# Kernel tuning notes

Hardware: AMD Instinct MI355X
Metric: run time of the kernel (lower is better)

Reference implementation:

```python
import jax, jax.numpy as jnp
import numpy as np

EPS = 1e-5

def conv3d(x, w):
    # x: [B,C,D,H,W], w: [O,I,3,3,3], stride 1, padding 1 (size preserving)
    return jax.lax.conv_general_dilated(
        x, w, window_strides=(1, 1, 1),
        padding=((1, 1), (1, 1), (1, 1)),
        dimension_numbers=('NCDHW', 'OIDHW', 'NCDHW'))

def deconv3d(x, w):
    # ConvTranspose3d(k=3, s=1, p=1) == conv3d with spatially flipped kernel, in/out swapped
    # torch ConvTranspose3d weight layout: [in, out, kD, kH, kW]
    wc = jnp.flip(w, axis=(2, 3, 4)).transpose(1, 0, 2, 3, 4)
    return conv3d(x, wc)

def batchnorm(x, bn):
    # bn: [4, C] rows = (gamma, beta, running_mean, running_var); inference mode
    g, b, m, v = bn[0], bn[1], bn[2], bn[3]
    scale = g * jax.lax.rsqrt(v + EPS)
    shift = b - m * scale
    return x * scale[None, :, None, None, None] + shift[None, :, None, None, None]

def qrnn_scan(Z, F, reverse):
    # gated linear recurrence h_t = f_t*h_{t-1} + (1-f_t)*z_t over depth axis (dim 2)
    Zs = jnp.moveaxis(Z, 2, 0)  # [D,B,C,H,W]
    Fs = jnp.moveaxis(F, 2, 0)
    def step(h, zf):
        z, f = zf
        h = f * h + (1.0 - f) * z
        return h, h
    h0 = jnp.zeros_like(Zs[0])  # h=None in torch == h=0 since f*0 vanishes
    _, hs = jax.lax.scan(step, h0, (Zs, Fs), reverse=reverse)
    return jnp.moveaxis(hs, 0, 2)

def qrnn_layer(x, w, bn, hidden, reverse, upsample, transpose):
    if upsample:
        # nn.Upsample(scale_factor=(1,2,2)) nearest
        x = jnp.repeat(jnp.repeat(x, 2, axis=3), 2, axis=4)
    g = deconv3d(x, w) if transpose else conv3d(x, w)
    g = batchnorm(g, bn)
    Z, F = g[:, :hidden], g[:, hidden:]
    return qrnn_scan(jnp.tanh(Z), jax.nn.sigmoid(F), reverse)

def setup_inputs():
    key = jax.random.key(0)
    ks = jax.random.split(key, 12)
    B, D = 4, 31
    x = jax.random.normal(ks[0], (B, 64, D, 32, 32), jnp.float32)
    xs2 = jax.random.normal(ks[1], (B, 32, D, 64, 64), jnp.float32)
    xs1 = jax.random.normal(ks[2], (B, 32, D, 64, 64), jnp.float32)
    xs0 = jax.random.normal(ks[3], (B, 16, D, 128, 128), jnp.float32)
    def wconv(k, shape):
        fan_in = shape[1] * 27
        return jax.random.normal(k, shape, jnp.float32) / np.float32(np.sqrt(fan_in))
    # layer0: UpsampleConv3d 64 -> 32 hidden (gates 64): Conv3d weight [64,64,3,3,3]
    w0 = wconv(ks[4], (64, 64, 3, 3, 3))
    # layer1: DeConv3D 32 -> 32 hidden (gates 64): ConvTranspose weight [in=32,out=64,3,3,3]
    w1 = wconv(ks[5], (32, 64, 3, 3, 3))
    # layer2: UpsampleConv3d 32 -> 16 hidden (gates 32): Conv3d weight [32,32,3,3,3]
    w2 = wconv(ks[6], (32, 32, 3, 3, 3))
    # layer3: DeConv3D 16 -> 16 hidden (gates 32): ConvTranspose weight [16,32,3,3,3]
    w3 = wconv(ks[7], (16, 32, 3, 3, 3))
    def mkbn(k, c):
        k1, k2, k3, k4 = jax.random.split(k, 4)
        return jnp.stack([
            jax.random.uniform(k1, (c,), jnp.float32, 0.5, 1.5),   # gamma
            jax.random.normal(k2, (c,), jnp.float32) * 0.1,        # beta
            jax.random.normal(k3, (c,), jnp.float32) * 0.1,        # running mean
            jax.random.uniform(k4, (c,), jnp.float32, 0.5, 1.5)])  # running var
    bn0 = mkbn(ks[8], 64)
    bn1 = mkbn(ks[9], 64)
    bn2 = mkbn(ks[10], 32)
    bn3 = mkbn(ks[11], 32)
    return dict(x=x, xs0=xs0, xs1=xs1, xs2=xs2,
                w0=w0, w1=w1, w2=w2, w3=w3,
                bn0=bn0, bn1=bn1, bn2=bn2, bn3=bn3)

def reference(x, xs0, xs1, xs2, w0, w1, w2, w3, bn0, bn1, bn2, bn3):
    # QRNN3DDecoder.forward with has_ad=True, reverse=False; scan direction alternates.
    # xs are popped last-first: xs2, xs1, xs0.
    h = qrnn_layer(x, w0, bn0, 32, False, True, False)          # upsample conv -> [B,32,D,64,64]
    h = qrnn_layer(h + xs2, w1, bn1, 32, True, False, True)     # deconv        -> [B,32,D,64,64]
    h = qrnn_layer(h + xs1, w2, bn2, 16, False, True, False)    # upsample conv -> [B,16,D,128,128]
    h = qrnn_layer(h + xs0, w3, bn3, 16, True, False, True)     # deconv        -> [B,16,D,128,128]
    return h
```

## Files before the change

kernel.cpp:

```cpp
#include <hip/hip_runtime.h>
#include <math.h>

#define BB 4
#define DD 31

typedef _Float16 half8 __attribute__((ext_vector_type(8)));
typedef float f32x4 __attribute__((ext_vector_type(4)));

__device__ __forceinline__ int swz(int b) { return b ^ (((b >> 7) & 7) << 4); }

__device__ __forceinline__ half8 ldswz(const _Float16* lin, int byteoff) {
    return *(const half8*)((const char*)lin + swz(byteoff));
}

__device__ __forceinline__ float fast_tanh(float y) {
    float e = __expf(2.f * y);
    return 1.f - 2.f * __builtin_amdgcn_rcpf(e + 1.f);
}
__device__ __forceinline__ float fast_sigmoid(float y) {
    return __builtin_amdgcn_rcpf(1.f + __expf(-y));
}


__global__ void bnprep(const float* __restrict__ bn, int C, float* __restrict__ sh) {
    int c = threadIdx.x;
    if (c >= C) return;
    float g = bn[c], b = bn[C + c], m = bn[2 * C + c], v = bn[3 * C + c];
    sh[c] = b - m * (g * rsqrtf(v + 1e-5f));
}

__global__ void wprep(const float* __restrict__ src, const float* __restrict__ bn,
                      _Float16* __restrict__ dst, int CIN, int COUT, int KS, int tr) {
    int idx = blockIdx.x * 256 + threadIdx.x;
    int total = KS * 32 * COUT;
    if (idx >= total) return;
    int ki = idx % 32;
    int co = (idx / 32) % COUT;
    int ko = idx / (32 * COUT);
    int k = ko * 32 + ki;
    float v = 0.f;
    if (k < 27 * CIN) {
        int tap = k / CIN, ci = k % CIN;
        v = tr ? src[((size_t)ci * COUT + co) * 27 + (26 - tap)]
               : src[((size_t)co * CIN + ci) * 27 + tap];
        v *= bn[co] * rsqrtf(bn[3 * COUT + co] + 1e-5f);
    }
    dst[((size_t)ko * COUT + co) * 32 + ki] = (_Float16)v;
}

__global__ void wprep_up(const float* __restrict__ src, const float* __restrict__ bn,
                         _Float16* __restrict__ dst, int CIN, int COUT) {
    const int KS = 12 * CIN / 32;
    int idx = blockIdx.x * 256 + threadIdx.x;
    int total = 4 * KS * 32 * COUT;
    if (idx >= total) return;
    int ki = idx % 32;
    int co = (idx / 32) % COUT;
    int ko = (idx / (32 * COUT)) % KS;
    int par = idx / (32 * COUT * KS);
    int k = ko * 32 + ki;
    int ci = k % CIN, tap = k / CIN;
    int kd = tap >> 2, ih = (tap >> 1) & 1, iw = tap & 1;
    int ph = par >> 1, pw = par & 1;
    const float c[2][2][3] = {{{1, 0, 0}, {0, 1, 1}}, {{1, 1, 0}, {0, 0, 1}}};
    float v = 0.f;
    for (int kh = 0; kh < 3; ++kh)
        for (int kw = 0; kw < 3; ++kw)
            v += c[ph][ih][kh] * c[pw][iw][kw] *
                 src[((size_t)co * CIN + ci) * 27 + kd * 9 + kh * 3 + kw];
    v *= bn[co] * rsqrtf(bn[3 * COUT + co] + 1e-5f);
    dst[(((size_t)par * KS + ko) * COUT + co) * 32 + ki] = (_Float16)v;
}

__global__ __launch_bounds__(256) void xconv(const float* __restrict__ src,
                                             _Float16* __restrict__ dst) {
    int idx = blockIdx.x * 256 + threadIdx.x;
    if (idx >= 4 * 31 * 1024 * 8) return;
    int cb = idx & 7;
    int pos = (idx >> 3) & 1023;
    int bd = idx >> 13;
    int d = bd % 31, b = bd / 31;
    half8 v;
#pragma unroll
    for (int j = 0; j < 8; ++j)
        v[j] = (_Float16)src[(((size_t)b * 64 + cb * 8 + j) * 31 + d) * 1024 + pos];
    *(half8*)(dst + ((size_t)bd * 1024 + pos) * 64 + cb * 8) = v;
}

template <int CIN, int COUT, int S, int KSTEPS>
__global__ __launch_bounds__(256, 2) void conv_mfma(
    const _Float16* __restrict__ inp,
    const _Float16* __restrict__ wq,
    const float* __restrict__ bnsh,
    _Float16* __restrict__ gout) {

    constexpr int IH = 18;
    constexpr int IW = 18;
    constexpr int NCB = COUT / 16;
    constexpr int NC8 = CIN / 8;
    constexpr int PATCH = 3 * IH * IW;

    __shared__ __align__(16) _Float16 lin[PATCH * CIN];

    const int tid = threadIdx.x;
    const int lane = tid & 63;
    const int wv = tid >> 6;
    const int col = lane & 15;
    const int grp = lane >> 4;

    const int w0 = blockIdx.x * 16;
    const int h0 = blockIdx.y * 16;
    const int bz = blockIdx.z;
    const int d = bz % DD;

    const int ibh = h0 - 1;
    const int ibw = w0 - 1;

    for (int idx = tid; idx < PATCH * NC8; idx += 256) {
        int c8 = idx % NC8;
        int pos = idx / NC8;
        int iw = pos % IW, t = pos / IW;
        int ih = t % IH, kd = t / IH;
        int dz = d + kd - 1, gh = ibh + ih, gw = ibw + iw;
        half8 v = {0, 0, 0, 0, 0, 0, 0, 0};
        if ((unsigned)dz < (unsigned)DD && (unsigned)gh < (unsigned)S &&
            (unsigned)gw < (unsigned)S)
            v = *(const half8*)(inp +
                (((size_t)(bz + kd - 1) * S + gh) * S + gw) * CIN + c8 * 8);
        *(half8*)((char*)lin + swz((pos * CIN + c8 * 8) * 2)) = v;
    }
    __syncthreads();

    f32x4 acc[4][NCB];
#pragma unroll
    for (int f = 0; f < 4; ++f)
#pragma unroll
        for (int n = 0; n < NCB; ++n) acc[f][n] = {0.f, 0.f, 0.f, 0.f};

#pragma unroll
    for (int ko = 0; ko < KSTEPS; ++ko) {
        int kd, kh, kw, ci;
        if (CIN >= 32) {
            int tap = (ko * 32) / CIN;
            kd = tap / 9; kh = (tap / 3) % 3; kw = tap % 3;
            ci = (ko * 32) % CIN + grp * 8;
        } else {
            int t0 = (2 * ko < 27) ? 2 * ko : 26;
            int t1 = (2 * ko + 1 < 27) ? 2 * ko + 1 : 26;
            int hi = grp >> 1;
            kd = hi ? t1 / 9 : t0 / 9;
            kh = hi ? (t1 / 3) % 3 : (t0 / 3) % 3;
            kw = hi ? t1 % 3 : t0 % 3;
            ci = (grp & 1) * 8;
        }

        half8 a[4];
        int iw = col + kw;
        int cb = ((kd * IH + wv * 4 + kh) * IW + iw) * CIN + ci;
#pragma unroll
        for (int f = 0; f < 4; ++f)
            a[f] = ldswz(lin, (cb + f * IW * CIN) * 2);

        half8 bfr[NCB];
#pragma unroll
        for (int n = 0; n < NCB; ++n)
            bfr[n] = *(const half8*)(wq + ((ko * COUT + n * 16 + col) * 32 + grp * 8));
#pragma unroll
        for (int f = 0; f < 4; ++f)
#pragma unroll
            for (int n = 0; n < NCB; ++n)
                acc[f][n] = __builtin_amdgcn_mfma_f32_16x16x32_f16(a[f], bfr[n],
                                                                   acc[f][n], 0, 0, 0);
    }

    const size_t obase = (size_t)bz * S * S * COUT;
#pragma unroll
    for (int n = 0; n < NCB; ++n) {
        int co = n * 16 + col;
        float sh = bnsh[co];
#pragma unroll
        for (int f = 0; f < 4; ++f) {
            int h = h0 + wv * 4 + f;
#pragma unroll
            for (int r = 0; r < 4; ++r) {
                int w = w0 + grp * 4 + r;
                float y = acc[f][n][r] + sh;
                float v = (n < NCB / 2) ? fast_tanh(y) : fast_sigmoid(y);
                gout[obase + ((size_t)h * S + w) * COUT + co] = (_Float16)v;
            }
        }
    }
}

template <int CIN, int COUT, int S, int MINW>
__global__ __launch_bounds__(256, MINW) void conv_up(
    const _Float16* __restrict__ inp,
    const _Float16* __restrict__ wqu,
    const float* __restrict__ bnsh,
    _Float16* __restrict__ gout) {

    constexpr int SIN = S / 2;
    constexpr int KS = 12 * CIN / 32;
    constexpr int NCB = COUT / 16;
    constexpr int NC8 = CIN / 8;
    constexpr int IH = 6, IW = 18;
    constexpr int PATCH = 3 * IH * IW;

    __shared__ __align__(16) _Float16 lin[PATCH * CIN];

    const int tid = threadIdx.x;
    const int lane = tid & 63;
    const int wv = tid >> 6;
    const int col = lane & 15;
    const int grp = lane >> 4;
    const int ph = wv >> 1, pw = wv & 1;

    const int bwp = blockIdx.x * 16;
    const int bhp = blockIdx.y * 4;
    const int bz = blockIdx.z;
    const int d = bz % DD;

    for (int idx = tid; idx < PATCH * NC8; idx += 256) {
        int c8 = idx % NC8;
        int pos = idx / NC8;
        int iwp = pos % IW, t = pos / IW;
        int ihp = t % IH, kd = t / IH;
        int dz = d + kd - 1, gh = bhp - 1 + ihp, gw = bwp - 1 + iwp;
        half8 v = {0, 0, 0, 0, 0, 0, 0, 0};
        if ((unsigned)dz < (unsigned)DD && (unsigned)gh < (unsigned)SIN &&
            (unsigned)gw < (unsigned)SIN)
            v = *(const half8*)(inp +
                (((size_t)(bz + kd - 1) * SIN + gh) * SIN + gw) * CIN + c8 * 8);
        *(half8*)((char*)lin + swz((pos * CIN + c8 * 8) * 2)) = v;
    }
    __syncthreads();

    f32x4 acc[4][NCB];
#pragma unroll
    for (int f = 0; f < 4; ++f)
#pragma unroll
        for (int n = 0; n < NCB; ++n) acc[f][n] = {0.f, 0.f, 0.f, 0.f};

    const _Float16* wqp = wqu + (size_t)(ph * 2 + pw) * KS * COUT * 32;

#pragma unroll
    for (int ko = 0; ko < KS; ++ko) {
        int tap = (ko * 32) / CIN;
        int ci = (ko * 32) % CIN + grp * 8;
        int kd = tap >> 2, ih = (tap >> 1) & 1, iwk = tap & 1;

        int lcol = col + iwk + pw;
        int r0 = ih + ph;
        int cb = ((kd * IH + r0) * IW + lcol) * CIN + ci;
        half8 a[4];
#pragma unroll
        for (int f = 0; f < 4; ++f)
            a[f] = ldswz(lin, (cb + f * IW * CIN) * 2);

        half8 bfr[NCB];
#pragma unroll
        for (int n = 0; n < NCB; ++n)
            bfr[n] = *(const half8*)(wqp + ((ko * COUT + n * 16 + col) * 32 + grp * 8));
#pragma unroll
        for (int f = 0; f < 4; ++f)
#pragma unroll
            for (int n = 0; n < NCB; ++n)
                acc[f][n] = __builtin_amdgcn_mfma_f32_16x16x32_f16(a[f], bfr[n],
                                                                   acc[f][n], 0, 0, 0);
    }

    const size_t obase = (size_t)bz * S * S * COUT;
#pragma unroll
    for (int n = 0; n < NCB; ++n) {
        int co = n * 16 + col;
        float sh = bnsh[co];
#pragma unroll
        for (int f = 0; f < 4; ++f) {
            int h = 2 * (bhp + f) + ph;
#pragma unroll
            for (int r = 0; r < 4; ++r) {
                int w = 2 * (bwp + grp * 4 + r) + pw;
                float y = acc[f][n][r] + sh;
                float v = (n < NCB / 2) ? fast_tanh(y) : fast_sigmoid(y);
                gout[obase + ((size_t)h * S + w) * COUT + co] = (_Float16)v;
            }
        }
    }
}

template <int H, int HW, int LAST>
__global__ __launch_bounds__(256) void qscan(
    const _Float16* __restrict__ g, const float* __restrict__ xs,
    _Float16* __restrict__ hout, float* __restrict__ fout, int rev) {
    constexpr int NCB = H / 8;
    int idx = blockIdx.x * 256 + threadIdx.x;
    if (idx >= BB * HW * NCB) return;
    int cb = idx % NCB;
    int hw = (idx / NCB) % HW;
    int b = idx / (NCB * HW);
    int c0 = cb * 8;

    float h[8];
#pragma unroll
    for (int j = 0; j < 8; ++j) h[j] = 0.f;

    for (int t = 0; t < DD; ++t) {
        int d = rev ? (DD - 1 - t) : t;
        const _Float16* gp = g + ((size_t)(b * DD + d) * HW + hw) * (2 * H);
        half8 z8 = *(const half8*)(gp + c0);
        half8 f8 = *(const half8*)(gp + H + c0);
        if (LAST) {
#pragma unroll
            for (int j = 0; j < 8; ++j) {
                float fv = (float)f8[j];
                h[j] = fv * h[j] + (1.f - fv) * (float)z8[j];
                fout[(((size_t)b * H + c0 + j) * DD + d) * HW + hw] = h[j];
            }
        } else {
            half8 o;
#pragma unroll
            for (int j = 0; j < 8; ++j) {
                float fv = (float)f8[j];
                h[j] = fv * h[j] + (1.f - fv) * (float)z8[j];
                o[j] = (_Float16)(h[j] + xs[(((size_t)b * H + c0 + j) * DD + d) * HW + hw]);
            }
            *(half8*)(hout + ((size_t)(b * DD + d) * HW + hw) * H + c0) = o;
        }
    }
}

extern "C" void kernel_launch(void* const* d_in, const int* in_sizes, int n_in,
                              void* d_out, int out_size, void* d_ws, size_t ws_size,
                              hipStream_t stream) {
    const float* x   = (const float*)d_in[0];
    const float* xs0 = (const float*)d_in[1];
    const float* xs1 = (const float*)d_in[2];
    const float* xs2 = (const float*)d_in[3];
    const float* w0  = (const float*)d_in[4];
    const float* w1  = (const float*)d_in[5];
    const float* w2  = (const float*)d_in[6];
    const float* w3  = (const float*)d_in[7];
    const float* bn0 = (const float*)d_in[8];
    const float* bn1 = (const float*)d_in[9];
    const float* bn2 = (const float*)d_in[10];
    const float* bn3 = (const float*)d_in[11];
    float* out = (float*)d_out;

    char* p = (char*)d_ws;
    _Float16* xf = (_Float16*)p;  p += (size_t)124 * 1024 * 64 * 2;
    _Float16* gA = (_Float16*)p;  p += (size_t)124 * 4096 * 64 * 2;
    _Float16* hA = (_Float16*)p;  p += (size_t)124 * 4096 * 32 * 2;
    _Float16* gB = (_Float16*)p;  p += (size_t)124 * 16384 * 32 * 2;
    _Float16* hB = (_Float16*)p;  p += (size_t)124 * 16384 * 16 * 2;
    _Float16* wqu0 = (_Float16*)p; p += (size_t)4 * 24 * 64 * 32 * 2;
    _Float16* wq1  = (_Float16*)p; p += 27 * 64 * 32 * 2;
    _Float16* wqu2 = (_Float16*)p; p += (size_t)4 * 12 * 32 * 32 * 2;
    _Float16* wq3  = (_Float16*)p; p += 14 * 32 * 32 * 2;
    float* sh0 = (float*)p;       p += 64 * 4;
    float* sh1 = (float*)p;       p += 64 * 4;
    float* sh2 = (float*)p;       p += 64 * 4;
    float* sh3 = (float*)p;       p += 64 * 4;

    xconv<<<(4 * 31 * 1024 * 8 + 255) / 256, 256, 0, stream>>>(x, xf);
    wprep_up<<<(4 * 24 * 32 * 64 + 255) / 256, 256, 0, stream>>>(w0, bn0, wqu0, 64, 64);
    wprep<<<(27 * 32 * 64 + 255) / 256, 256, 0, stream>>>(w1, bn1, wq1, 32, 64, 27, 1);
    wprep_up<<<(4 * 12 * 32 * 32 + 255) / 256, 256, 0, stream>>>(w2, bn2, wqu2, 32, 32);
    wprep<<<(14 * 32 * 32 + 255) / 256, 256, 0, stream>>>(w3, bn3, wq3, 16, 32, 14, 1);
    bnprep<<<1, 64, 0, stream>>>(bn0, 64, sh0);
    bnprep<<<1, 64, 0, stream>>>(bn1, 64, sh1);
    bnprep<<<1, 64, 0, stream>>>(bn2, 32, sh2);
    bnprep<<<1, 64, 0, stream>>>(bn3, 32, sh3);

    conv_up<64, 64, 64, 3><<<dim3(2, 8, BB * DD), 256, 0, stream>>>(xf, wqu0, sh0, gA);
    qscan<32, 4096, 0><<<(BB * 4096 * 4 + 255) / 256, 256, 0, stream>>>(gA, xs2, hA, nullptr, 0);

    conv_mfma<32, 64, 64, 27><<<dim3(4, 4, BB * DD), 256, 0, stream>>>(hA, wq1, sh1, gA);
    qscan<32, 4096, 0><<<(BB * 4096 * 4 + 255) / 256, 256, 0, stream>>>(gA, xs1, hA, nullptr, 1);

    conv_up<32, 32, 128, 4><<<dim3(4, 16, BB * DD), 256, 0, stream>>>(hA, wqu2, sh2, gB);
    qscan<16, 16384, 0><<<(BB * 16384 * 2 + 255) / 256, 256, 0, stream>>>(gB, xs0, hB, nullptr, 0);

    conv_mfma<16, 32, 128, 14><<<dim3(8, 8, BB * DD), 256, 0, stream>>>(hB, wq3, sh3, gB);
    qscan<16, 16384, 1><<<(BB * 16384 * 2 + 255) / 256, 256, 0, stream>>>(gB, nullptr, nullptr, out, 1);
}
```

Measured before the change: 567.1 us.

## Fuse QRNN depth scan into conv kernels with rolling depth-plane LDS buffer

Each conv kernel now walks the whole depth axis for its spatial tile and output-channel slice, keeping the recurrent state in registers and applying tanh/sigmoid, the gated recurrence and the skip-add inline. This removes the separate qscan kernels and the round trip of the gate tensors through global memory. Input planes are staged in a 4-slot rolling LDS ring, with the next plane prefetched into registers during the MFMA work. Weights are re-laid out so each block reads only its channel slice. The cost is far fewer blocks per launch (the depth dimension leaves the grid) and a serial dependency across depth, which lowers parallelism and occupancy.

Result: slower. 602.8 us (+6.3%).

```diff
diff --git a/kernel.cpp b/kernel.cpp
--- a/kernel.cpp
+++ b/kernel.cpp
@@ -8,11 +8,12 @@
 typedef float f32x4 __attribute__((ext_vector_type(4)));
 
 __device__ __forceinline__ int swz(int b) { return b ^ (((b >> 7) & 7) << 4); }
-
 __device__ __forceinline__ half8 ldswz(const _Float16* lin, int byteoff) {
     return *(const half8*)((const char*)lin + swz(byteoff));
 }
-
+__device__ __forceinline__ void stswz(_Float16* lin, int byteoff, half8 v) {
+    *(half8*)((char*)lin + swz(byteoff)) = v;
+}
 __device__ __forceinline__ float fast_tanh(float y) {
     float e = __expf(2.f * y);
     return 1.f - 2.f * __builtin_amdgcn_rcpf(e + 1.f);
@@ -30,13 +31,16 @@
 }
 
 __global__ void wprep(const float* __restrict__ src, const float* __restrict__ bn,
-                      _Float16* __restrict__ dst, int CIN, int COUT, int KS, int tr) {
+                      _Float16* __restrict__ dst, int CIN, int COUT, int KS, int CS, int tr) {
     int idx = blockIdx.x * 256 + threadIdx.x;
-    int total = KS * 32 * COUT;
+    int total = CS * KS * 1024;
     if (idx >= total) return;
-    int ki = idx % 32;
-    int co = (idx / 32) % COUT;
-    int ko = idx / (32 * COUT);
+    int ki = idx & 31;
+    int c16 = (idx >> 5) & 15;
+    int n = (idx >> 9) & 1;
+    int ko = (idx >> 10) % KS;
+    int q = idx / (KS * 1024);
+    int co = n * (COUT / 2) + q * 16 + c16;
     int k = ko * 32 + ki;
     float v = 0.f;
     if (k < 27 * CIN) {
@@ -45,19 +49,21 @@
                : src[((size_t)co * CIN + ci) * 27 + tap];
         v *= bn[co] * rsqrtf(bn[3 * COUT + co] + 1e-5f);
     }
-    dst[((size_t)ko * COUT + co) * 32 + ki] = (_Float16)v;
+    dst[idx] = (_Float16)v;
 }
 
 __global__ void wprep_up(const float* __restrict__ src, const float* __restrict__ bn,
-                         _Float16* __restrict__ dst, int CIN, int COUT) {
-    const int KS = 12 * CIN / 32;
+                         _Float16* __restrict__ dst, int CIN, int COUT, int KS, int CS) {
     int idx = blockIdx.x * 256 + threadIdx.x;
-    int total = 4 * KS * 32 * COUT;
+    int total = CS * 4 * KS * 1024;
     if (idx >= total) return;
-    int ki = idx % 32;
-    int co = (idx / 32) % COUT;
-    int ko = (idx / (32 * COUT)) % KS;
-    int par = idx / (32 * COUT * KS);
+    int ki = idx & 31;
+    int c16 = (idx >> 5) & 15;
+    int n = (idx >> 9) & 1;
+    int ko = (idx >> 10) % KS;
+    int par = (idx / (KS * 1024)) & 3;
+    int q = idx / (KS * 4096);
+    int co = n * (COUT / 2) + q * 16 + c16;
     int k = ko * 32 + ki;
     int ci = k % CIN, tap = k / CIN;
     int kd = tap >> 2, ih = (tap >> 1) & 1, iw = tap & 1;
@@ -69,7 +75,7 @@
             v += c[ph][ih][kh] * c[pw][iw][kw] *
                  src[((size_t)co * CIN + ci) * 27 + kd * 9 + kh * 3 + kw];
     v *= bn[co] * rsqrtf(bn[3 * COUT + co] + 1e-5f);
-    dst[(((size_t)par * KS + ko) * COUT + co) * 32 + ki] = (_Float16)v;
+    dst[idx] = (_Float16)v;
 }
 
 __global__ __launch_bounds__(256) void xconv(const float* __restrict__ src,
@@ -87,20 +93,24 @@
     *(half8*)(dst + ((size_t)bd * 1024 + pos) * 64 + cb * 8) = v;
 }
 
-template <int CIN, int COUT, int S, int KSTEPS>
-__global__ __launch_bounds__(256, 2) void conv_mfma(
+template <int CIN, int S, int HID, int KS, int NF, int CS, int REV, int LAST>
+__global__ __launch_bounds__(256, 2) void fconv(
     const _Float16* __restrict__ inp,
     const _Float16* __restrict__ wq,
     const float* __restrict__ bnsh,
-    _Float16* __restrict__ gout) {
-
-    constexpr int IH = 18;
+    const float* __restrict__ xs,
+    _Float16* __restrict__ hout,
+    float* __restrict__ fout) {
+
     constexpr int IW = 18;
-    constexpr int NCB = COUT / 16;
+    constexpr int TH = 4 * NF;
+    constexpr int IHP = TH + 2;
     constexpr int NC8 = CIN / 8;
-    constexpr int PATCH = 3 * IH * IW;
-
-    __shared__ __align__(16) _Float16 lin[PATCH * CIN];
+    constexpr int P8 = IHP * IW * NC8;
+    constexpr int NST = (P8 + 255) / 256;
+    constexpr int PLANEB = IHP * IW * CIN * 2;
+
+    __shared__ __align__(16) _Float16 lin[4 * IHP * IW * CIN];
 
     const int tid = threadIdx.x;
     const int lane = tid & 63;
@@ -109,104 +119,158 @@
     const int grp = lane >> 4;
 
     const int w0 = blockIdx.x * 16;
-    const int h0 = blockIdx.y * 16;
-    const int bz = blockIdx.z;
-    const int d = bz % DD;
-
-    const int ibh = h0 - 1;
-    const int ibw = w0 - 1;
-
-    for (int idx = tid; idx < PATCH * NC8; idx += 256) {
-        int c8 = idx % NC8;
-        int pos = idx / NC8;
-        int iw = pos % IW, t = pos / IW;
-        int ih = t % IH, kd = t / IH;
-        int dz = d + kd - 1, gh = ibh + ih, gw = ibw + iw;
-        half8 v = {0, 0, 0, 0, 0, 0, 0, 0};
-        if ((unsigned)dz < (unsigned)DD && (unsigned)gh < (unsigned)S &&
-            (unsigned)gw < (unsigned)S)
-            v = *(const half8*)(inp +
-                (((size_t)(bz + kd - 1) * S + gh) * S + gw) * CIN + c8 * 8);
-        *(half8*)((char*)lin + swz((pos * CIN + c8 * 8) * 2)) = v;
-    }
+    const int h0 = blockIdx.y * TH;
+    const int b = blockIdx.z / CS;
+    const int q = blockIdx.z % CS;
+    const size_t bbase = (size_t)b * DD;
+
+    const float shz = bnsh[q * 16 + col];
+    const float shf = bnsh[HID + q * 16 + col];
+    const int hc = q * 16 + col;
+    const _Float16* wqb = wq + (size_t)q * KS * 1024;
+
+    auto stage_now = [&](int dz) {
+        int slot = (dz + 8) & 3;
+        for (int idx = tid; idx < P8; idx += 256) {
+            int c8 = idx % NC8;
+            int pos = idx / NC8;
+            int ih = pos / IW, iw = pos % IW;
+            int gh = h0 - 1 + ih, gw = w0 - 1 + iw;
+            half8 v = {0, 0, 0, 0, 0, 0, 0, 0};
+            if ((unsigned)dz < (unsigned)DD && (unsigned)gh < (unsigned)S &&
+                (unsigned)gw < (unsigned)S)
+                v = *(const half8*)(inp + (((bbase + dz) * S + gh) * S + gw) * CIN + c8 * 8);
+            stswz(lin, slot * PLANEB + (pos * CIN + c8 * 8) * 2, v);
+        }
+    };
+
+    constexpr int dir = REV ? -1 : 1;
+    const int d0 = REV ? DD - 1 : 0;
+    stage_now(d0 - dir);
+    stage_now(d0);
+    stage_now(d0 + dir);
     __syncthreads();
 
-    f32x4 acc[4][NCB];
-#pragma unroll
-    for (int f = 0; f < 4; ++f)
-#pragma unroll
-        for (int n = 0; n < NCB; ++n) acc[f][n] = {0.f, 0.f, 0.f, 0.f};
-
-#pragma unroll
-    for (int ko = 0; ko < KSTEPS; ++ko) {
-        int kd, kh, kw, ci;
-        if (CIN >= 32) {
-            int tap = (ko * 32) / CIN;
-            kd = tap / 9; kh = (tap / 3) % 3; kw = tap % 3;
-            ci = (ko * 32) % CIN + grp * 8;
-        } else {
-            int t0 = (2 * ko < 27) ? 2 * ko : 26;
-            int t1 = (2 * ko + 1 < 27) ? 2 * ko + 1 : 26;
-            int hi = grp >> 1;
-            kd = hi ? t1 / 9 : t0 / 9;
-            kh = hi ? (t1 / 3) % 3 : (t0 / 3) % 3;
-            kw = hi ? t1 % 3 : t0 % 3;
-            ci = (grp & 1) * 8;
-        }
-
-        half8 a[4];
-        int iw = col + kw;
-        int cb = ((kd * IH + wv * 4 + kh) * IW + iw) * CIN + ci;
-#pragma unroll
-        for (int f = 0; f < 4; ++f)
-            a[f] = ldswz(lin, (cb + f * IW * CIN) * 2);
-
-        half8 bfr[NCB];
-#pragma unroll
-        for (int n = 0; n < NCB; ++n)
-            bfr[n] = *(const half8*)(wq + ((ko * COUT + n * 16 + col) * 32 + grp * 8));
-#pragma unroll
-        for (int f = 0; f < 4; ++f)
-#pragma unroll
-            for (int n = 0; n < NCB; ++n)
-                acc[f][n] = __builtin_amdgcn_mfma_f32_16x16x32_f16(a[f], bfr[n],
-                                                                   acc[f][n], 0, 0, 0);
-    }
-
-    const size_t obase = (size_t)bz * S * S * COUT;
-#pragma unroll
-    for (int n = 0; n < NCB; ++n) {
-        int co = n * 16 + col;
-        float sh = bnsh[co];
-#pragma unroll
-        for (int f = 0; f < 4; ++f) {
-            int h = h0 + wv * 4 + f;
+    float hst[NF][4];
+#pragma unroll
+    for (int f = 0; f < NF; ++f)
+#pragma unroll
+        for (int r = 0; r < 4; ++r) hst[f][r] = 0.f;
+
+    for (int t = 0; t < DD; ++t) {
+        const int d = d0 + dir * t;
+        const int dzl = d + 2 * dir;
+
+        half8 sv[NST];
+#pragma unroll
+        for (int i = 0; i < NST; ++i) {
+            int idx = tid + i * 256;
+            half8 v = {0, 0, 0, 0, 0, 0, 0, 0};
+            if (idx < P8) {
+                int c8 = idx % NC8;
+                int pos = idx / NC8;
+                int ih = pos / IW, iw = pos % IW;
+                int gh = h0 - 1 + ih, gw = w0 - 1 + iw;
+                if ((unsigned)dzl < (unsigned)DD && (unsigned)gh < (unsigned)S &&
+                    (unsigned)gw < (unsigned)S)
+                    v = *(const half8*)(inp +
+                        (((bbase + dzl) * S + gh) * S + gw) * CIN + c8 * 8);
+            }
+            sv[i] = v;
+        }
+
+        f32x4 acc[NF][2];
+#pragma unroll
+        for (int f = 0; f < NF; ++f) {
+            acc[f][0] = {0.f, 0.f, 0.f, 0.f};
+            acc[f][1] = {0.f, 0.f, 0.f, 0.f};
+        }
+#pragma unroll
+        for (int ko = 0; ko < KS; ++ko) {
+            int kd, kh, kw, ci;
+            if (CIN >= 32) {
+                int tap = (ko * 32) / CIN;
+                kd = tap / 9; kh = (tap / 3) % 3; kw = tap % 3;
+                ci = (ko * 32) % CIN + grp * 8;
+            } else {
+                int t0 = (2 * ko < 27) ? 2 * ko : 26;
+                int t1 = (2 * ko + 1 < 27) ? 2 * ko + 1 : 26;
+                int hi = grp >> 1;
+                kd = hi ? t1 / 9 : t0 / 9;
+                kh = hi ? (t1 / 3) % 3 : (t0 / 3) % 3;
+                kw = hi ? t1 % 3 : t0 % 3;
+                ci = (grp & 1) * 8;
+            }
+            int slot = (d + kd + 7) & 3;
+            int iw = col + kw;
+            half8 a[NF];
+#pragma unroll
+            for (int f = 0; f < NF; ++f)
+                a[f] = ldswz(lin, slot * PLANEB +
+                             (((wv * NF + f + kh) * IW + iw) * CIN + ci) * 2);
+            half8 bf0 = *(const half8*)(wqb + ko * 1024 + col * 32 + grp * 8);
+            half8 bf1 = *(const half8*)(wqb + ko * 1024 + 512 + col * 32 + grp * 8);
+#pragma unroll
+            for (int f = 0; f < NF; ++f) {
+                acc[f][0] = __builtin_amdgcn_mfma_f32_16x16x32_f16(a[f], bf0, acc[f][0], 0, 0, 0);
+                acc[f][1] = __builtin_amdgcn_mfma_f32_16x16x32_f16(a[f], bf1, acc[f][1], 0, 0, 0);
+            }
+        }
+
+        {
+            int slot = (dzl + 8) & 3;
+#pragma unroll
+            for (int i = 0; i < NST; ++i) {
+                int idx = tid + i * 256;
+                if (idx < P8) {
+                    int c8 = idx % NC8;
+                    int pos = idx / NC8;
+                    stswz(lin, slot * PLANEB + (pos * CIN + c8 * 8) * 2, sv[i]);
+                }
+            }
+        }
+
+#pragma unroll
+        for (int f = 0; f < NF; ++f) {
+            int h = h0 + wv * NF + f;
 #pragma unroll
             for (int r = 0; r < 4; ++r) {
                 int w = w0 + grp * 4 + r;
-                float y = acc[f][n][r] + sh;
-                float v = (n < NCB / 2) ? fast_tanh(y) : fast_sigmoid(y);
-                gout[obase + ((size_t)h * S + w) * COUT + co] = (_Float16)v;
-            }
-        }
+                size_t sp = (size_t)h * S + w;
+                float z = fast_tanh(acc[f][0][r] + shz);
+                float fg = fast_sigmoid(acc[f][1][r] + shf);
+                hst[f][r] = fg * hst[f][r] + (1.f - fg) * z;
+                if (LAST) {
+                    fout[(((size_t)b * HID + hc) * DD + d) * ((size_t)S * S) + sp] = hst[f][r];
+                } else {
+                    float xv = xs[(((size_t)b * HID + hc) * DD + d) * ((size_t)S * S) + sp];
+                    hout[((bbase + d) * ((size_t)S * S) + sp) * HID + hc] =
+                        (_Float16)(hst[f][r] + xv);
+                }
+            }
+        }
+        __syncthreads();
     }
 }
 
-template <int CIN, int COUT, int S, int MINW>
-__global__ __launch_bounds__(256, MINW) void conv_up(
+template <int CIN, int S, int HID, int KS, int NF, int CS, int REV, int LAST>
+__global__ __launch_bounds__(256, 2) void fconv_up(
     const _Float16* __restrict__ inp,
-    const _Float16* __restrict__ wqu,
+    const _Float16* __restrict__ wq,
     const float* __restrict__ bnsh,
-    _Float16* __restrict__ gout) {
+    const float* __restrict__ xs,
+    _Float16* __restrict__ hout,
+    float* __restrict__ fout) {
 
     constexpr int SIN = S / 2;
-    constexpr int KS = 12 * CIN / 32;
-    constexpr int NCB = COUT / 16;
+    constexpr int IW = 18;
+    constexpr int IHP = NF + 2;
     constexpr int NC8 = CIN / 8;
-    constexpr int IH = 6, IW = 18;
-    constexpr int PATCH = 3 * IH * IW;
-
-    __shared__ __align__(16) _Float16 lin[PATCH * CIN];
+    constexpr int P8 = IHP * IW * NC8;
+    constexpr int NST = (P8 + 255) / 256;
+    constexpr int PLANEB = IHP * IW * CIN * 2;
+
+    __shared__ __align__(16) _Float16 lin[4 * IHP * IW * CIN];
 
     const int tid = threadIdx.x;
     const int lane = tid & 63;
@@ -216,116 +280,127 @@
     const int ph = wv >> 1, pw = wv & 1;
 
     const int bwp = blockIdx.x * 16;
-    const int bhp = blockIdx.y * 4;
-    const int bz = blockIdx.z;
-    const int d = bz % DD;
-
-    for (int idx = tid; idx < PATCH * NC8; idx += 256) {
-        int c8 = idx % NC8;
-        int pos = idx / NC8;
-        int iwp = pos % IW, t = pos / IW;
-        int ihp = t % IH, kd = t / IH;
-        int dz = d + kd - 1, gh = bhp - 1 + ihp, gw = bwp - 1 + iwp;
-        half8 v = {0, 0, 0, 0, 0, 0, 0, 0};
-        if ((unsigned)dz < (unsigned)DD && (unsigned)gh < (unsigned)SIN &&
-            (unsigned)gw < (unsigned)SIN)
-            v = *(const half8*)(inp +
-                (((size_t)(bz + kd - 1) * SIN + gh) * SIN + gw) * CIN + c8 * 8);
-        *(half8*)((char*)lin + swz((pos * CIN + c8 * 8) * 2)) = v;
-    }
+    const int bhp = blockIdx.y * NF;
+    const int b = blockIdx.z / CS;
+    const int q = blockIdx.z % CS;
+    const size_t bbase = (size_t)b * DD;
+
+    const float shz = bnsh[q * 16 + col];
+    const float shf = bnsh[HID + q * 16 + col];
+    const int hc = q * 16 + col;
+    const _Float16* wqb = wq + ((size_t)(q * 4 + wv) * KS) * 1024;
+
+    auto stage_now = [&](int dz) {
+        int slot = (dz + 8) & 3;
+        for (int idx = tid; idx < P8; idx += 256) {
+            int c8 = idx % NC8;
+            int pos = idx / NC8;
+            int ih = pos / IW, iw = pos % IW;
+            int gh = bhp - 1 + ih, gw = bwp - 1 + iw;
+            half8 v = {0, 0, 0, 0, 0, 0, 0, 0};
+            if ((unsigned)dz < (unsigned)DD && (unsigned)gh < (unsigned)SIN &&
+                (unsigned)gw < (unsigned)SIN)
+                v = *(const half8*)(inp + (((bbase + dz) * SIN + gh) * SIN + gw) * CIN + c8 * 8);
+            stswz(lin, slot * PLANEB + (pos * CIN + c8 * 8) * 2, v);
+        }
+    };
+
+    constexpr int dir = REV ? -1 : 1;
+    const int d0 = REV ? DD - 1 : 0;
+    stage_now(d0 - dir);
+    stage_now(d0);
+    stage_now(d0 + dir);
     __syncthreads();
 
-    f32x4 acc[4][NCB];
-#pragma unroll
-    for (int f = 0; f < 4; ++f)
-#pragma unroll
-        for (int n = 0; n < NCB; ++n) acc[f][n] = {0.f, 0.f, 0.f, 0.f};
-
-    const _Float16* wqp = wqu + (size_t)(ph * 2 + pw) * KS * COUT * 32;
-
-#pragma unroll
-    for (int ko = 0; ko < KS; ++ko) {
-        int tap = (ko * 32) / CIN;
-        int ci = (ko * 32) % CIN + grp * 8;
-        int kd = tap >> 2, ih = (tap >> 1) & 1, iwk = tap & 1;
-
-        int lcol = col + iwk + pw;
-        int r0 = ih + ph;
-        int cb = ((kd * IH + r0) * IW + lcol) * CIN + ci;
-        half8 a[4];
-#pragma unroll
-        for (int f = 0; f < 4; ++f)
-            a[f] = ldswz(lin, (cb + f * IW * CIN) * 2);
-
-        half8 bfr[NCB];
-#pragma unroll
-        for (int n = 0; n < NCB; ++n)
-            bfr[n] = *(const half8*)(wqp + ((ko * COUT + n * 16 + col) * 32 + grp * 8));
-#pragma unroll
-        for (int f = 0; f < 4; ++f)
-#pragma unroll
-            for (int n = 0; n < NCB; ++n)
-                acc[f][n] = __builtin_amdgcn_mfma_f32_16x16x32_f16(a[f], bfr[n],
-                                                                   acc[f][n], 0, 0, 0);
-    }
-
-    const size_t obase = (size_t)bz * S * S * COUT;
-#pragma unroll
-    for (int n = 0; n < NCB; ++n) {
-        int co = n * 16 + col;
-        float sh = bnsh[co];
-#pragma unroll
-        for (int f = 0; f < 4; ++f) {
+    float hst[NF][4];
+#pragma unroll
+    for (int f = 0; f < NF; ++f)
+#pragma unroll
+        for (int r = 0; r < 4; ++r) hst[f][r] = 0.f;
+
+    for (int t = 0; t < DD; ++t) {
+        const int d = d0 + dir * t;
+        const int dzl = d + 2 * dir;
+
+        half8 sv[NST];
+#pragma unroll
+        for (int i = 0; i < NST; ++i) {
+            int idx = tid + i * 256;
+            half8 v = {0, 0, 0, 0, 0, 0, 0, 0};
+            if (idx < P8) {
+                int c8 = idx % NC8;
+                int pos = idx / NC8;
+                int ih = pos / IW, iw = pos % IW;
+                int gh = bhp - 1 + ih, gw = bwp - 1 + iw;
+                if ((unsigned)dzl < (unsigned)DD && (unsigned)gh < (unsigned)SIN &&
+                    (unsigned)gw < (unsigned)SIN)
+                    v = *(const half8*)(inp +
+                        (((bbase + dzl) * SIN + gh) * SIN + gw) * CIN + c8 * 8);
+            }
+            sv[i] = v;
+        }
+
+        f32x4 acc[NF][2];
+#pragma unroll
+        for (int f = 0; f < NF; ++f) {
+            acc[f][0] = {0.f, 0.f, 0.f, 0.f};
+            acc[f][1] = {0.f, 0.f, 0.f, 0.f};
+        }
+#pragma unroll
+        for (int ko = 0; ko < KS; ++ko) {
+            int tap = (ko * 32) / CIN;
+            int ci = (ko * 32) % CIN + grp * 8;
+            int kd = tap >> 2, ihh = (tap >> 1) & 1, iwk = tap & 1;
+            int slot = (d + kd + 7) & 3;
+            int lcol = col + iwk + pw;
+            int row0 = ihh + ph;
+            half8 a[NF];
+#pragma unroll
+            for (int f = 0; f < NF; ++f)
+                a[f] = ldswz(lin, slot * PLANEB +
+                             ((((row0 + f) * IW) + lcol) * CIN + ci) * 2);
+            half8 bf0 = *(const half8*)(wqb + ko * 1024 + col * 32 + grp * 8);
+            half8 bf1 = *(const half8*)(wqb + ko * 1024 + 512 + col * 32 + grp * 8);
+#pragma unroll
+            for (int f = 0; f < NF; ++f) {
+                acc[f][0] = __builtin_amdgcn_mfma_f32_16x16x32_f16(a[f], bf0, acc[f][0], 0, 0, 0);
+                acc[f][1] = __builtin_amdgcn_mfma_f32_16x16x32_f16(a[f], bf1, acc[f][1], 0, 0, 0);
+            }
+        }
+
+        {
+            int slot = (dzl + 8) & 3;
+#pragma unroll
+            for (int i = 0; i < NST; ++i) {
+                int idx = tid + i * 256;
+                if (idx < P8) {
+                    int c8 = idx % NC8;
+                    int pos = idx / NC8;
+                    stswz(lin, slot * PLANEB + (pos * CIN + c8 * 8) * 2, sv[i]);
+                }
+            }
+        }
+
+#pragma unroll
+        for (int f = 0; f < NF; ++f) {
             int h = 2 * (bhp + f) + ph;
 #pragma unroll
             for (int r = 0; r < 4; ++r) {
                 int w = 2 * (bwp + grp * 4 + r) + pw;
-                float y = acc[f][n][r] + sh;
-                float v = (n < NCB / 2) ? fast_tanh(y) : fast_sigmoid(y);
-                gout[obase + ((size_t)h * S + w) * COUT + co] = (_Float16)v;
-            }
-        }
-    }
-}
-
-template <int H, int HW, int LAST>
-__global__ __launch_bounds__(256) void qscan(
-    const _Float16* __restrict__ g, const float* __restrict__ xs,
-    _Float16* __restrict__ hout, float* __restrict__ fout, int rev) {
-    constexpr int NCB = H / 8;
-    int idx = blockIdx.x * 256 + threadIdx.x;
-    if (idx >= BB * HW * NCB) return;
-    int cb = idx % NCB;
-    int hw = (idx / NCB) % HW;
-    int b = idx / (NCB * HW);
-    int c0 = cb * 8;
-
-    float h[8];
-#pragma unroll
-    for (int j = 0; j < 8; ++j) h[j] = 0.f;
-
-    for (int t = 0; t < DD; ++t) {
-        int d = rev ? (DD - 1 - t) : t;
-        const _Float16* gp = g + ((size_t)(b * DD + d) * HW + hw) * (2 * H);
-        half8 z8 = *(const half8*)(gp + c0);
-        half8 f8 = *(const half8*)(gp + H + c0);
-        if (LAST) {
-#pragma unroll
-            for (int j = 0; j < 8; ++j) {
-                float fv = (float)f8[j];
-                h[j] = fv * h[j] + (1.f - fv) * (float)z8[j];
-                fout[(((size_t)b * H + c0 + j) * DD + d) * HW + hw] = h[j];
-            }
-        } else {
-            half8 o;
-#pragma unroll
-            for (int j = 0; j < 8; ++j) {
-                float fv = (float)f8[j];
-                h[j] = fv * h[j] + (1.f - fv) * (float)z8[j];
-                o[j] = (_Float16)(h[j] + xs[(((size_t)b * H + c0 + j) * DD + d) * HW + hw]);
-            }
-            *(half8*)(hout + ((size_t)(b * DD + d) * HW + hw) * H + c0) = o;
-        }
+                size_t sp = (size_t)h * S + w;
+                float z = fast_tanh(acc[f][0][r] + shz);
+                float fg = fast_sigmoid(acc[f][1][r] + shf);
+                hst[f][r] = fg * hst[f][r] + (1.f - fg) * z;
+                if (LAST) {
+                    fout[(((size_t)b * HID + hc) * DD + d) * ((size_t)S * S) + sp] = hst[f][r];
+                } else {
+                    float xv = xs[(((size_t)b * HID + hc) * DD + d) * ((size_t)S * S) + sp];
+                    hout[((bbase + d) * ((size_t)S * S) + sp) * HID + hc] =
+                        (_Float16)(hst[f][r] + xv);
+                }
+            }
+        }
+        __syncthreads();
     }
 }
 
@@ -347,39 +422,35 @@
     float* out = (float*)d_out;
 
     char* p = (char*)d_ws;
-    _Float16* xf = (_Float16*)p;  p += (size_t)124 * 1024 * 64 * 2;
-    _Float16* gA = (_Float16*)p;  p += (size_t)124 * 4096 * 64 * 2;
-    _Float16* hA = (_Float16*)p;  p += (size_t)124 * 4096 * 32 * 2;
-    _Float16* gB = (_Float16*)p;  p += (size_t)124 * 16384 * 32 * 2;
-    _Float16* hB = (_Float16*)p;  p += (size_t)124 * 16384 * 16 * 2;
-    _Float16* wqu0 = (_Float16*)p; p += (size_t)4 * 24 * 64 * 32 * 2;
-    _Float16* wq1  = (_Float16*)p; p += 27 * 64 * 32 * 2;
-    _Float16* wqu2 = (_Float16*)p; p += (size_t)4 * 12 * 32 * 32 * 2;
-    _Float16* wq3  = (_Float16*)p; p += 14 * 32 * 32 * 2;
-    float* sh0 = (float*)p;       p += 64 * 4;
-    float* sh1 = (float*)p;       p += 64 * 4;
-    float* sh2 = (float*)p;       p += 64 * 4;
-    float* sh3 = (float*)p;       p += 64 * 4;
+    _Float16* xf   = (_Float16*)p; p += (size_t)124 * 1024 * 64 * 2;
+    _Float16* hA   = (_Float16*)p; p += (size_t)124 * 4096 * 32 * 2;
+    _Float16* hA2  = (_Float16*)p; p += (size_t)124 * 4096 * 32 * 2;
+    _Float16* hB   = (_Float16*)p; p += (size_t)124 * 16384 * 16 * 2;
+    _Float16* wq0u = (_Float16*)p; p += (size_t)2 * 4 * 24 * 1024 * 2;
+    _Float16* wq1  = (_Float16*)p; p += (size_t)2 * 27 * 1024 * 2;
+    _Float16* wq2u = (_Float16*)p; p += (size_t)4 * 12 * 1024 * 2;
+    _Float16* wq3  = (_Float16*)p; p += (size_t)14 * 1024 * 2;
+    float* sh0 = (float*)p; p += 64 * 4;
+    float* sh1 = (float*)p; p += 64 * 4;
+    float* sh2 = (float*)p; p += 64 * 4;
+    float* sh3 = (float*)p; p += 64 * 4;
 
     xconv<<<(4 * 31 * 1024 * 8 + 255) / 256, 256, 0, stream>>>(x, xf);
-    wprep_up<<<(4 * 24 * 32 * 64 + 255) / 256, 256, 0, stream>>>(w0, bn0, wqu0, 64, 64);
-    wprep<<<(27 * 32 * 64 + 255) / 256, 256, 0, stream>>>(w1, bn1, wq1, 32, 64, 27, 1);
-    wprep_up<<<(4 * 12 * 32 * 32 + 255) / 256, 256, 0, stream>>>(w2, bn2, wqu2, 32, 32);
-    wprep<<<(14 * 32 * 32 + 255) / 256, 256, 0, stream>>>(w3, bn3, wq3, 16, 32, 14, 1);
+    wprep_up<<<(2 * 4 * 24 * 1024 + 255) / 256, 256, 0, stream>>>(w0, bn0, wq0u, 64, 64, 24, 2);
+    wprep<<<(2 * 27 * 1024 + 255) / 256, 256, 0, stream>>>(w1, bn1, wq1, 32, 64, 27, 2, 1);
+    wprep_up<<<(4 * 12 * 1024 + 255) / 256, 256, 0, stream>>>(w2, bn2, wq2u, 32, 32, 12, 1);
+    wprep<<<(14 * 1024 + 255) / 256, 256, 0, stream>>>(w3, bn3, wq3, 16, 32, 14, 1, 1);
     bnprep<<<1, 64, 0, stream>>>(bn0, 64, sh0);
     bnprep<<<1, 64, 0, stream>>>(bn1, 64, sh1);
     bnprep<<<1, 64, 0, stream>>>(bn2, 32, sh2);
     bnprep<<<1, 64, 0, stream>>>(bn3, 32, sh3);
 
-    conv_up<64, 64, 64, 3><<<dim3(2, 8, BB * DD), 256, 0, stream>>>(xf, wqu0, sh0, gA);
-    qscan<32, 4096, 0><<<(BB * 4096 * 4 + 255) / 256, 256, 0, stream>>>(gA, xs2, hA, nullptr, 0);
-
-    conv_mfma<32, 64, 64, 27><<<dim3(4, 4, BB * DD), 256, 0, stream>>>(hA, wq1, sh1, gA);
-    qscan<32, 4096, 0><<<(BB * 4096 * 4 + 255) / 256, 256, 0, stream>>>(gA, xs1, hA, nullptr, 1);
-
-    conv_up<32, 32, 128, 4><<<dim3(4, 16, BB * DD), 256, 0, stream>>>(hA, wqu2, sh2, gB);
-    qscan<16, 16384, 0><<<(BB * 16384 * 2 + 255) / 256, 256, 0, stream>>>(gB, xs0, hB, nullptr, 0);
-
-    conv_mfma<16, 32, 128, 14><<<dim3(8, 8, BB * DD), 256, 0, stream>>>(hB, wq3, sh3, gB);
-    qscan<16, 16384, 1><<<(BB * 16384 * 2 + 255) / 256, 256, 0, stream>>>(gB, nullptr, nullptr, out, 1);
-}
+    fconv_up<64, 64, 32, 24, 1, 2, 0, 0><<<dim3(2, 32, BB * 2), 256, 0, stream>>>(
+        xf, wq0u, sh0, xs2, hA, nullptr);
+    fconv<32, 64, 32, 27, 1, 2, 1, 0><<<dim3(4, 16, BB * 2), 256, 0, stream>>>(
+        hA, wq1, sh1, xs1, hA2, nullptr);
+    fconv_up<32, 128, 16, 12, 2, 1, 0, 0><<<dim3(4, 32, BB), 256, 0, stream>>>(
+        hA2, wq2u, sh2, xs0, hB, nullptr);
+    fconv<16, 128, 16, 14, 2, 1, 1, 1><<<dim3(8, 16, BB), 256, 0, stream>>>(
+        hB, wq3, sh3, nullptr, nullptr, out);
+}
```
